# Kernel optimization log

Measured on AMD Instinct MI355X. Metric: run time of the kernel, lower is better.

The kernel has to match this reference:

```python
import jax, jax.numpy as jnp
import numpy as np
from jax import lax

# Module hyper-parameters (match init_kwargs)
NUM_IN = 8       # num_input_capsules
IN_DIM = 16      # input_capsule_dimension
K = 5            # kernel_size (padding=2 => 'same' spatial size)
PAD = 2
NUM_OUT = 8      # num_output_capsules
OUT_DIM = 16     # output_capsules_dimension
ROUTING = 3


def squash(p):
    # p: [..., D]; squash along last dim (matches torch squash with 1e-9 eps)
    p_norm_sq = jnp.sum(p * p, axis=-1, keepdims=True)
    p_norm = jnp.sqrt(p_norm_sq + 1e-9)
    return p_norm_sq / (1.0 + p_norm_sq) * p / p_norm


def setup_inputs() -> dict:
    key = jax.random.key(0)
    k1, k2 = jax.random.split(key)
    N, H, W_sp = 8, 64, 64
    u = jax.random.normal(k1, (N, NUM_IN, IN_DIM, H, W_sp), dtype=jnp.float32)
    # per-input-capsule conv weights, scaled ~1/sqrt(fan_in) for numerical sanity
    W = jax.random.normal(k2, (NUM_IN, NUM_OUT * OUT_DIM, IN_DIM, K, K), dtype=jnp.float32) * 0.05
    return {"u": u, "W": W}


def _forward(u, W):
    N = u.shape[0]

    def conv_one(x, w):  # x: [N,Cin,H,W], w: [OD,Cin,K,K]
        return lax.conv_general_dilated(x, w, window_strides=(1, 1),
                                        padding=[(PAD, PAD), (PAD, PAD)],
                                        dimension_numbers=('NCHW', 'OIHW', 'NCHW'))

    # vmap over the input-capsule axis (each capsule has its own conv)
    u_hat = jax.vmap(conv_one, in_axes=(1, 0))(u, W)          # [I, N, O*D, H, W]
    H, W_sp = u_hat.shape[-2], u_hat.shape[-1]
    u_hat = u_hat.reshape(NUM_IN, N, NUM_OUT, OUT_DIM, H, W_sp)
    u_hat = u_hat.transpose(0, 1, 4, 5, 2, 3)                 # [I, N, H, W, O, D]

    spatial_pad = [(0, 0), (0, 0), (0, 0), (PAD, PAD), (PAD, PAD)]
    b = jnp.zeros((NUM_IN, N, NUM_OUT, H, W_sp), dtype=u_hat.dtype)

    v = None
    for d in range(ROUTING):
        uh = u_hat if d == ROUTING - 1 else lax.stop_gradient(u_hat)
        # local spatial max (KxK, stride 1, -inf pad) then max over output capsules
        b_sp_max = lax.reduce_window(b, -jnp.inf, lax.max,
                                     (1, 1, 1, K, K), (1, 1, 1, 1, 1), spatial_pad)
        b_max = jnp.max(b_sp_max, axis=2, keepdims=True)      # [I, N, 1, H, W]
        c = jnp.exp(b - b_max)                                # [I, N, O, H, W]
        # conv2d_same with all-ones [1,O,K,K] kernel == sum over O and KxK window
        sum_c = lax.reduce_window(c, 0.0, lax.add,
                                  (1, 1, NUM_OUT, K, K), (1, 1, 1, 1, 1), spatial_pad)
        r = c / sum_c                                         # [I, N, O, H, W]
        r_nhwo = r.transpose(0, 1, 3, 4, 2)                   # [I, N, H, W, O]
        p = jnp.einsum('inhwo,inhwod->nhwod', r_nhwo, uh)     # sum over input capsules
        v = squash(p)                                         # [N, H, W, O, D]
        if d < ROUTING - 1:
            agree = jnp.einsum('inhwod,nhwod->inhwo', uh, v)  # [I, N, H, W, O]
            b = b + agree.transpose(0, 1, 4, 2, 3)            # back to [I, N, O, H, W]
    # final transpose_(1,3).transpose_(2,4): [N,H,W,O,D] -> [N,O,D,H,W]
    return v.transpose(0, 3, 4, 1, 2)


def reference(u, W):
    return _forward(u, W)
```

## Files before the change

kernel.cpp:

```cpp
#include <hip/hip_runtime.h>
#include <hip/hip_fp16.h>
#include <cmath>

#define HWS 4096
#define HWP 2048

typedef _Float16 f16x8 __attribute__((ext_vector_type(8)));
typedef float f32x16 __attribute__((ext_vector_type(16)));
typedef unsigned short ushort_t;
typedef ushort_t ushort8 __attribute__((ext_vector_type(8)));
typedef unsigned int uint_t;

static constexpr size_t UHP_OFF = 0;
static constexpr size_t B_OFF   = 16777216ull;
static constexpr size_t WGT_OFF = 18874368ull;
static constexpr size_t WPK_OFF = 20971520ull;

__device__ __forceinline__ float h2f(uint_t u) { return __half2float(__ushort_as_half((ushort_t)u)); }

__global__ __launch_bounds__(256) void wpack_kernel(const float* __restrict__ W,
                                                    ushort_t* __restrict__ wp) {
  const int gid = blockIdx.x * 256 + threadIdx.x;
  const int lane = gid & 63;
  int r = gid >> 6;
  const int oct = r & 3; r >>= 2;
  const int tap = r % 25, i = r / 25;
  const int oc = oct * 32 + (lane & 31);
  const int cin0 = (lane >> 5) * 8;
  ushort8 out;
#pragma unroll
  for (int e = 0; e < 8; ++e) {
    float f = W[(((size_t)i * 128 + oc) * 16 + cin0 + e) * 25 + tap];
    out[e] = __half_as_ushort(__float2half(f));
  }
  *(ushort8*)(wp + (size_t)gid * 8) = out;
}

__global__ __launch_bounds__(512, 4) void conv_kernel(const float* __restrict__ u,
                                                      const ushort_t* __restrict__ wp,
                                                      uint_t* __restrict__ uhp) {
  __shared__ ushort_t ut[8 * 68 * 24];

  const int tid = threadIdx.x;
  const int lane = tid & 63, wid = tid >> 6;
  const int l31 = lane & 31, half = lane >> 5;
  const int wv = wid >> 1, oh = wid & 1;
  const int h0 = blockIdx.x * 4;
  const int q = blockIdx.y;
  const int i = q & 7, n = q >> 3;

  const ushort_t* wbase = wp + (size_t)i * 51200 + (oh * 2) * 512 + lane * 8;
  uint4 bcur[2], bnxt[2];
#pragma unroll
  for (int f = 0; f < 2; ++f) bcur[f] = *(const uint4*)(wbase + f * 512);

  const float* ub = u + (size_t)q * 16 * HWS;
  {
    const int lane_x = tid & 63;
    const int grp = tid >> 6;
    const int gh = h0 - 2 + grp;
    const bool rowok = (unsigned)gh < 64u;
    const float* src = ub + gh * 64 + lane_x;
    float vals[16];
#pragma unroll
    for (int it = 0; it < 16; ++it)
      vals[it] = rowok ? src[(size_t)it * HWS] : 0.f;
    const int xbase = (grp * 68 + lane_x + 2) * 24;
#pragma unroll
    for (int itp = 0; itp < 8; ++itp) {
      uint_t pk = (uint_t)__half_as_ushort(__float2half(vals[2 * itp])) |
                  ((uint_t)__half_as_ushort(__float2half(vals[2 * itp + 1])) << 16);
      *(uint_t*)&ut[xbase + 2 * itp] = pk;
    }
    if (tid < 256) {
      const int y = tid >> 5, r = tid & 31;
      const int xs = r >> 3, cp = r & 7;
      const int x = (xs < 2) ? xs : (64 + xs);
      *(uint_t*)&ut[(y * 68 + x) * 24 + 2 * cp] = 0u;
    }
  }
  __syncthreads();

  f32x16 acc[2][2];
#pragma unroll
  for (int pt = 0; pt < 2; ++pt)
#pragma unroll
    for (int ot = 0; ot < 2; ++ot)
#pragma unroll
      for (int e = 0; e < 16; ++e) acc[pt][ot][e] = 0.f;

  for (int tap = 0; tap < 25; ++tap) {
    const int kh = tap / 5, kw = tap - kh * 5;
    if (tap < 24) {
      const ushort_t* nb = wbase + (tap + 1) * 2048;
#pragma unroll
      for (int f = 0; f < 2; ++f) bnxt[f] = *(const uint4*)(nb + f * 512);
    }
    f16x8 ah[2];
#pragma unroll
    for (int pt = 0; pt < 2; ++pt)
      ah[pt] = *(const f16x8*)&ut[((wv + kh) * 68 + pt * 32 + l31 + kw) * 24 + half * 8];
#pragma unroll
    for (int ot = 0; ot < 2; ++ot) {
      f16x8 bb = *(const f16x8*)&bcur[ot];
#pragma unroll
      for (int pt = 0; pt < 2; ++pt)
        acc[pt][ot] = __builtin_amdgcn_mfma_f32_32x32x16_f16(ah[pt], bb, acc[pt][ot], 0, 0, 0);
    }
#pragma unroll
    for (int f = 0; f < 2; ++f) bcur[f] = bnxt[f];
  }

  const int h = h0 + wv;
  uint_t* uhb = uhp + ((size_t)(n * HWP + h * 32) * 8 + i) * 128;
#pragma unroll
  for (int pt = 0; pt < 2; ++pt)
#pragma unroll
    for (int ot = 0; ot < 2; ++ot) {
      const int otg = oh * 2 + ot;
#pragma unroll
      for (int rp = 0; rp < 8; ++rp) {
        const int r = rp * 2;
        const int xp = pt * 16 + 4 * (rp >> 1) + 2 * half + (rp & 1);
        uint_t lo = (uint_t)__half_as_ushort(__float2half(acc[pt][ot][r]));
        uint_t hi = (uint_t)__half_as_ushort(__float2half(acc[pt][ot][r + 1]));
        uhb[(size_t)xp * 1024 + otg * 32 + l31] = lo | (hi << 16);
      }
    }
}

__global__ __launch_bounds__(256) void fsm_kernel(const float* __restrict__ b,
                                                  float* __restrict__ wgt) {
  __shared__ float bt[8][36][36];
  __shared__ float m1[40][40];
  __shared__ float bm[36][36];
  __shared__ float st[36][36];
  const int tid = threadIdx.x;
  const int i = blockIdx.z >> 3, n = blockIdx.z & 7;
  const int h0 = blockIdx.y * 32, w0 = blockIdx.x * 32;
  const int inb = i * 8 + n;
  const float* bb = b + (size_t)inb * HWS * 8;

  for (int idx = tid; idx < 1600; idx += 256) {
    const int yy = idx / 40, xx = idx - yy * 40;
    const int h = h0 + yy - 4, w = w0 + xx - 4;
    float v[8];
    if ((unsigned)h < 64u && (unsigned)w < 64u) {
      const float4 a = *(const float4*)(bb + (size_t)(h * 64 + w) * 8);
      const float4 c = *(const float4*)(bb + (size_t)(h * 64 + w) * 8 + 4);
      v[0] = a.x; v[1] = a.y; v[2] = a.z; v[3] = a.w;
      v[4] = c.x; v[5] = c.y; v[6] = c.z; v[7] = c.w;
    } else {
#pragma unroll
      for (int o = 0; o < 8; ++o) v[o] = -INFINITY;
    }
    float m = v[0];
#pragma unroll
    for (int o = 1; o < 8; ++o) m = fmaxf(m, v[o]);
    m1[yy][xx] = m;
    if ((unsigned)(yy - 2) < 36u && (unsigned)(xx - 2) < 36u) {
#pragma unroll
      for (int o = 0; o < 8; ++o) bt[o][yy - 2][xx - 2] = v[o];
    }
  }
  __syncthreads();
  for (int idx = tid; idx < 1296; idx += 256) {
    const int ys = idx / 36, xs = idx - ys * 36;
    float m = -INFINITY;
#pragma unroll
    for (int dy = 0; dy < 5; ++dy)
#pragma unroll
      for (int dx = 0; dx < 5; ++dx) m = fmaxf(m, m1[ys + dy][xs + dx]);
    bm[ys][xs] = m;
  }
  __syncthreads();
  for (int idx = tid; idx < 1296; idx += 256) {
    const int ys = idx / 36, xs = idx - ys * 36;
    const float bmv = bm[ys][xs];
    float ss = 0.f;
#pragma unroll
    for (int o = 0; o < 8; ++o) ss += __expf(bt[o][ys][xs] - bmv);
    st[ys][xs] = ss;
  }
  __syncthreads();
  const int tx = tid & 31, ty = tid >> 5;
  for (int p = 0; p < 4; ++p) {
    const int y = ty + p * 8, x = tx;
    float sum = 0.f;
#pragma unroll
    for (int dy = 0; dy < 5; ++dy)
#pragma unroll
      for (int dx = 0; dx < 5; ++dx) sum += st[y + dy][x + dx];
    const float rs = 1.0f / sum;
    const float bmv = bm[y + 2][x + 2];
    float w8[8];
#pragma unroll
    for (int o = 0; o < 8; ++o) w8[o] = __expf(bt[o][y + 2][x + 2] - bmv) * rs;
    float* dst = wgt + (size_t)inb * HWS * 8 + (size_t)((h0 + y) * 64 + (w0 + x)) * 8;
    *(float4*)dst = make_float4(w8[0], w8[1], w8[2], w8[3]);
    *(float4*)(dst + 4) = make_float4(w8[4], w8[5], w8[6], w8[7]);
  }
}

template <int INIT, int FINAL>
__global__ __launch_bounds__(256) void route_kernel(const uint_t* __restrict__ uhp,
                                                    const float* __restrict__ wgt,
                                                    float* __restrict__ b,
                                                    float* __restrict__ out) {
  __shared__ float sm_w[1024];
  __shared__ float sm_b[2048];
  const int tid = threadIdx.x;
  const int quad = tid & 31, slot = tid >> 5;
  const int o = quad >> 2;
  const int n = blockIdx.y;
  const int hw0 = blockIdx.x * 16;
  const int hwp = blockIdx.x * 8 + slot;

  if (!INIT) {
    const int li = tid >> 5, r = tid & 31;
    const int pxl = r >> 1, o4 = (r & 1) * 4;
    const float4 wv4 = *(const float4*)(wgt + ((size_t)(li * 8 + n) * HWS + hw0 + pxl) * 8 + o4);
    *(float4*)&sm_w[(li * 16 + pxl) * 8 + o4] = wv4;
    __syncthreads();
  }

  float uv0[8][4], uv1[8][4];
  float pa0[4] = {0.f, 0.f, 0.f, 0.f}, pa1[4] = {0.f, 0.f, 0.f, 0.f};
  const uint_t* up = uhp + (size_t)(n * HWP + hwp) * 1024 + quad * 4;
#pragma unroll
  for (int i = 0; i < 8; ++i) {
    const uint4 q4 = *(const uint4*)(up + i * 128);
    const uint_t qq[4] = {q4.x, q4.y, q4.z, q4.w};
    float w0 = 1.f, w1 = 1.f;
    if (!INIT) {
      w0 = sm_w[(i * 16 + slot * 2) * 8 + o];
      w1 = sm_w[(i * 16 + slot * 2 + 1) * 8 + o];
    }
#pragma unroll
    for (int e = 0; e < 4; ++e) {
      const float a0 = h2f(qq[e] & 0xffffu);
      const float a1 = h2f(qq[e] >> 16);
      uv0[i][e] = a0;
      uv1[i][e] = a1;
      pa0[e] = fmaf(w0, a0, pa0[e]);
      pa1[e] = fmaf(w1, a1, pa1[e]);
    }
  }
  if (INIT) {
    const int hwa = hw0 + slot * 2;
    const int h = hwa >> 6, x = hwa & 63;
    const int nh = min(h + 2, 63) - max(h - 2, 0) + 1;
    const int nw0 = min(x + 2, 63) - max(x - 2, 0) + 1;
    const int nw1 = min(x + 3, 63) - max(x - 1, 0) + 1;
    const float r0 = 1.0f / (float)(8 * nh * nw0);
    const float r1 = 1.0f / (float)(8 * nh * nw1);
#pragma unroll
    for (int e = 0; e < 4; ++e) { pa0[e] *= r0; pa1[e] *= r1; }
  }
  float ns0 = pa0[0] * pa0[0] + pa0[1] * pa0[1] + pa0[2] * pa0[2] + pa0[3] * pa0[3];
  float ns1 = pa1[0] * pa1[0] + pa1[1] * pa1[1] + pa1[2] * pa1[2] + pa1[3] * pa1[3];
  ns0 += __shfl_xor(ns0, 1); ns0 += __shfl_xor(ns0, 2);
  ns1 += __shfl_xor(ns1, 1); ns1 += __shfl_xor(ns1, 2);
  const float f0 = ns0 / ((1.f + ns0) * sqrtf(ns0 + 1e-9f));
  const float f1 = ns1 / ((1.f + ns1) * sqrtf(ns1 + 1e-9f));
  float v0[4], v1[4];
#pragma unroll
  for (int e = 0; e < 4; ++e) { v0[e] = f0 * pa0[e]; v1[e] = f1 * pa1[e]; }

  if (FINAL) {
#pragma unroll
    for (int e = 0; e < 4; ++e) {
      sm_b[(quad * 4 + e) * 16 + slot * 2] = v0[e];
      sm_b[(quad * 4 + e) * 16 + slot * 2 + 1] = v1[e];
    }
    __syncthreads();
    const int od = tid >> 1, p8 = (tid & 1) * 8;
    float* dst = out + ((size_t)n * 128 + od) * HWS + hw0 + p8;
    const float* src = &sm_b[od * 16 + p8];
    *(float4*)dst = make_float4(src[0], src[1], src[2], src[3]);
    *(float4*)(dst + 4) = make_float4(src[4], src[5], src[6], src[7]);
  } else {
#pragma unroll
    for (int i = 0; i < 8; ++i) {
      float a0 = uv0[i][0] * v0[0] + uv0[i][1] * v0[1] + uv0[i][2] * v0[2] + uv0[i][3] * v0[3];
      float a1 = uv1[i][0] * v1[0] + uv1[i][1] * v1[1] + uv1[i][2] * v1[2] + uv1[i][3] * v1[3];
      a0 += __shfl_xor(a0, 1); a0 += __shfl_xor(a0, 2);
      a1 += __shfl_xor(a1, 1); a1 += __shfl_xor(a1, 2);
      if ((quad & 3) == 0) {
        sm_b[(i * 16 + slot * 2) * 8 + o] = a0;
        sm_b[(i * 16 + slot * 2 + 1) * 8 + o] = a1;
      }
    }
    __syncthreads();
    const int li = tid >> 5, r = tid & 31;
    const int pxl = r >> 1, o4 = (r & 1) * 4;
    float* bp = b + ((size_t)(li * 8 + n) * HWS + hw0 + pxl) * 8 + o4;
    const float4 ag = *(const float4*)&sm_b[(li * 16 + pxl) * 8 + o4];
    if (INIT) {
      *(float4*)bp = ag;
    } else {
      float4 old = *(const float4*)bp;
      *(float4*)bp = make_float4(old.x + ag.x, old.y + ag.y, old.z + ag.z, old.w + ag.w);
    }
  }
}

extern "C" void kernel_launch(void* const* d_in, const int* in_sizes, int n_in,
                              void* d_out, int out_size, void* d_ws, size_t ws_size,
                              hipStream_t stream) {
  const float* u = (const float*)d_in[0];
  const float* W = (const float*)d_in[1];
  float* ws = (float*)d_ws;
  uint_t* uhp = (uint_t*)(ws + UHP_OFF);
  float* b = ws + B_OFF;
  float* wgt = ws + WGT_OFF;
  ushort_t* wpk = (ushort_t*)(ws + WPK_OFF);
  float* out = (float*)d_out;

  wpack_kernel<<<dim3(200), 256, 0, stream>>>(W, wpk);
  conv_kernel<<<dim3(16, 64), 512, 0, stream>>>(u, wpk, uhp);
  route_kernel<1, 0><<<dim3(256, 8), 256, 0, stream>>>(uhp, wgt, b, out);
  fsm_kernel<<<dim3(2, 2, 64), 256, 0, stream>>>(b, wgt);
  route_kernel<0, 0><<<dim3(256, 8), 256, 0, stream>>>(uhp, wgt, b, out);
  fsm_kernel<<<dim3(2, 2, 64), 256, 0, stream>>>(b, wgt);
  route_kernel<0, 1><<<dim3(256, 8), 256, 0, stream>>>(uhp, wgt, b, out);
}
```

Measured before the change: 111.1 us.

## Stage conv weights in shared memory and split output channels across blocks

The conv kernel now splits each block's work so every wave handles one pixel tile and two output tiles. Grid is doubled, with each block covering half of the output channels. All 25 taps of that block's weight slice are preloaded into LDS, replacing per-tap global prefetch into registers, and the tap loop is fully unrolled. This cuts accumulator registers and global weight traffic per wave. In exchange the input tile is loaded and converted twice and LDS use grows to about 76KB, which may limit occupancy.

```diff
diff --git a/kernel.cpp b/kernel.cpp
--- a/kernel.cpp
+++ b/kernel.cpp
@@ -40,19 +40,28 @@
                                                       const ushort_t* __restrict__ wp,
                                                       uint_t* __restrict__ uhp) {
   __shared__ ushort_t ut[8 * 68 * 24];
+  __shared__ ushort_t wt[25 * 1024];
 
   const int tid = threadIdx.x;
   const int lane = tid & 63, wid = tid >> 6;
   const int l31 = lane & 31, half = lane >> 5;
-  const int wv = wid >> 1, oh = wid & 1;
-  const int h0 = blockIdx.x * 4;
+  const int wv = wid >> 1, pt = wid & 1;
+  const int hb = blockIdx.x >> 1, oh = blockIdx.x & 1;
+  const int h0 = hb * 4;
   const int q = blockIdx.y;
   const int i = q & 7, n = q >> 3;
 
-  const ushort_t* wbase = wp + (size_t)i * 51200 + (oh * 2) * 512 + lane * 8;
-  uint4 bcur[2], bnxt[2];
-#pragma unroll
-  for (int f = 0; f < 2; ++f) bcur[f] = *(const uint4*)(wbase + f * 512);
+  {
+    const ushort_t* wsrc = wp + (size_t)i * 51200 + oh * 1024;
+#pragma unroll
+    for (int c = 0; c < 7; ++c) {
+      const int idx = c * 512 + tid;
+      if (idx < 3200) {
+        const int tap = idx >> 7, off = idx & 127;
+        *(uint4*)&wt[tap * 1024 + off * 8] = *(const uint4*)(wsrc + tap * 2048 + off * 8);
+      }
+    }
+  }
 
   const float* ub = u + (size_t)q * 16 * HWS;
   {
@@ -81,52 +90,36 @@
   }
   __syncthreads();
 
-  f32x16 acc[2][2];
-#pragma unroll
-  for (int pt = 0; pt < 2; ++pt)
-#pragma unroll
-    for (int ot = 0; ot < 2; ++ot)
-#pragma unroll
-      for (int e = 0; e < 16; ++e) acc[pt][ot][e] = 0.f;
-
+  f32x16 acc[2];
+#pragma unroll
+  for (int ot = 0; ot < 2; ++ot)
+#pragma unroll
+    for (int e = 0; e < 16; ++e) acc[ot][e] = 0.f;
+
+#pragma unroll
   for (int tap = 0; tap < 25; ++tap) {
     const int kh = tap / 5, kw = tap - kh * 5;
-    if (tap < 24) {
-      const ushort_t* nb = wbase + (tap + 1) * 2048;
-#pragma unroll
-      for (int f = 0; f < 2; ++f) bnxt[f] = *(const uint4*)(nb + f * 512);
-    }
-    f16x8 ah[2];
-#pragma unroll
-    for (int pt = 0; pt < 2; ++pt)
-      ah[pt] = *(const f16x8*)&ut[((wv + kh) * 68 + pt * 32 + l31 + kw) * 24 + half * 8];
-#pragma unroll
-    for (int ot = 0; ot < 2; ++ot) {
-      f16x8 bb = *(const f16x8*)&bcur[ot];
-#pragma unroll
-      for (int pt = 0; pt < 2; ++pt)
-        acc[pt][ot] = __builtin_amdgcn_mfma_f32_32x32x16_f16(ah[pt], bb, acc[pt][ot], 0, 0, 0);
-    }
-#pragma unroll
-    for (int f = 0; f < 2; ++f) bcur[f] = bnxt[f];
+    const f16x8 ah = *(const f16x8*)&ut[((wv + kh) * 68 + pt * 32 + l31 + kw) * 24 + half * 8];
+    const f16x8 b0 = *(const f16x8*)&wt[tap * 1024 + lane * 8];
+    const f16x8 b1 = *(const f16x8*)&wt[tap * 1024 + 512 + lane * 8];
+    acc[0] = __builtin_amdgcn_mfma_f32_32x32x16_f16(ah, b0, acc[0], 0, 0, 0);
+    acc[1] = __builtin_amdgcn_mfma_f32_32x32x16_f16(ah, b1, acc[1], 0, 0, 0);
   }
 
   const int h = h0 + wv;
   uint_t* uhb = uhp + ((size_t)(n * HWP + h * 32) * 8 + i) * 128;
 #pragma unroll
-  for (int pt = 0; pt < 2; ++pt)
-#pragma unroll
-    for (int ot = 0; ot < 2; ++ot) {
-      const int otg = oh * 2 + ot;
-#pragma unroll
-      for (int rp = 0; rp < 8; ++rp) {
-        const int r = rp * 2;
-        const int xp = pt * 16 + 4 * (rp >> 1) + 2 * half + (rp & 1);
-        uint_t lo = (uint_t)__half_as_ushort(__float2half(acc[pt][ot][r]));
-        uint_t hi = (uint_t)__half_as_ushort(__float2half(acc[pt][ot][r + 1]));
-        uhb[(size_t)xp * 1024 + otg * 32 + l31] = lo | (hi << 16);
-      }
-    }
+  for (int ot = 0; ot < 2; ++ot) {
+    const int otg = oh * 2 + ot;
+#pragma unroll
+    for (int rp = 0; rp < 8; ++rp) {
+      const int r = rp * 2;
+      const int xp = pt * 16 + 4 * (rp >> 1) + 2 * half + (rp & 1);
+      uint_t lo = (uint_t)__half_as_ushort(__float2half(acc[ot][r]));
+      uint_t hi = (uint_t)__half_as_ushort(__float2half(acc[ot][r + 1]));
+      uhb[(size_t)xp * 1024 + otg * 32 + l31] = lo | (hi << 16);
+    }
+  }
 }
 
 __global__ __launch_bounds__(256) void fsm_kernel(const float* __restrict__ b,
@@ -318,7 +311,7 @@
   float* out = (float*)d_out;
 
   wpack_kernel<<<dim3(200), 256, 0, stream>>>(W, wpk);
-  conv_kernel<<<dim3(16, 64), 512, 0, stream>>>(u, wpk, uhp);
+  conv_kernel<<<dim3(32, 64), 512, 0, stream>>>(u, wpk, uhp);
   route_kernel<1, 0><<<dim3(256, 8), 256, 0, stream>>>(uhp, wgt, b, out);
   fsm_kernel<<<dim3(2, 2, 64), 256, 0, stream>>>(b, wgt);
   route_kernel<0, 0><<<dim3(256, 8), 256, 0, stream>>>(uhp, wgt, b, out);
```

Result: slower. 120.4 us (+8.4%).
